# Performance work log

Hardware: AMD Instinct MI355X
Metric: run time of the kernel (lower is better)

Reference implementation:

```python
import jax, jax.numpy as jnp
import numpy as np

NUM_KERNELS = 301
GAMMA = 10.0
SHIFT = float(np.log(2.0))


def shifted_softplus(x):
    return jax.nn.softplus(x) - SHIFT


def setup_inputs() -> dict:
    key = jax.random.key(0)
    k1, k2, k3, k4, k5, k6 = jax.random.split(key, 6)
    N, F, K = 768, 128, NUM_KERNELS
    x = jax.random.normal(k1, (N, F), dtype=jnp.float32)
    # positions scaled to span a realistic distance range vs centers in [0, 30]
    r = jax.random.uniform(k2, (N, 3), dtype=jnp.float32) * 10.0
    W1 = jax.random.normal(k3, (K, F), dtype=jnp.float32) * (1.0 / np.sqrt(K))
    b1 = jax.random.normal(k4, (F,), dtype=jnp.float32) * 0.01
    W2 = jax.random.normal(k5, (F, F), dtype=jnp.float32) * (1.0 / np.sqrt(F))
    b2 = jax.random.normal(k6, (F,), dtype=jnp.float32) * 0.01
    return {"x": x, "r": r, "W1": W1, "b1": b1, "W2": W2, "b2": b2}


def reference(x, r, W1, b1, W2, b2):
    # pairwise Euclidean distances, safe at the zero diagonal
    diff = r[:, None, :] - r[None, :, :]            # [N, N, 3]
    sq = jnp.sum(diff * diff, axis=-1)              # [N, N]
    d = jnp.where(sq > 0, jnp.sqrt(jnp.where(sq > 0, sq, 1.0)), 0.0)
    centers = jnp.linspace(0.0, 30.0, NUM_KERNELS, dtype=jnp.float32)  # [K]
    expanded = jnp.exp(-GAMMA * jnp.square(d[..., None] - centers))    # [N, N, K]
    h = shifted_softplus(expanded @ W1 + b1)        # [N, N, F]
    w = shifted_softplus(h @ W2 + b2)               # [N, N, F]
    o = jnp.einsum('jk,ijk->ik', x, w)              # [N, F]
    return o
```

## Files before the change

### kernel.cpp

```cpp
#include <hip/hip_runtime.h>

#define F        128
#define NN       768
#define KE       192
#define E_STRIDE 200
#define H_STRIDE 136
#define NT       48
#define NBLK     (NT*(NT+1)/2)

#define L2E 1.44269504f
#define LN2 0.69314718f

typedef __attribute__((ext_vector_type(8))) short short8;
typedef __attribute__((ext_vector_type(4))) float floatx4;

__device__ __forceinline__ unsigned short f2bf(float f) {
    union { float f; unsigned u; } v; v.f = f;
    return (unsigned short)((v.u + 0x8000u) >> 16);
}

__device__ __forceinline__ float ssp_zl(float zl2e) {
    float t = exp2f(zl2e);
    float u = __log2f(1.0f + t);
    return fmaf(LN2, u, -LN2);
}

__device__ __forceinline__ void pin(short8& v) { asm volatile("" : "+v"(v)); }

__global__ void prep_w(const float* __restrict__ W1, const float* __restrict__ W2,
                       unsigned short* __restrict__ W1s, unsigned short* __restrict__ W2s,
                       float* __restrict__ out) {
    int idx = blockIdx.x * 256 + threadIdx.x;
    out[idx] = 0.0f;
    if (idx < KE * F) {
        int t = idx & 7, lane = (idx >> 3) & 63, frag = idx >> 9;
        int k = (frag >> 3) * 32 + (lane >> 4) * 8 + t;
        int n = (frag & 7) * 16 + (lane & 15);
        W1s[idx] = f2bf(W1[k * F + n]);
    } else if (idx < KE * F + F * F) {
        int j = idx - KE * F;
        int t = j & 7, lane = (j >> 3) & 63, frag = j >> 9;
        int k = (frag >> 3) * 32 + (lane >> 4) * 8 + t;
        int n = (frag & 7) * 16 + (lane & 15);
        W2s[j] = f2bf(W2[k * F + n]);
    }
}

__global__ __launch_bounds__(256, 2) void cfconv_main(
    const float* __restrict__ x, const float* __restrict__ r,
    const float* __restrict__ b1, const float* __restrict__ b2,
    const unsigned short* __restrict__ W1s, const unsigned short* __restrict__ W2s,
    float* __restrict__ out)
{
    __shared__ __align__(16) unsigned short e_lds[64 * E_STRIDE];
    __shared__ __align__(16) unsigned short h_lds[64 * H_STRIDE];
    __shared__ float d_all[256];
    __shared__ int   klo_all[256];

    const int tid  = threadIdx.x;
    const int lane = tid & 63;
    const int wave = tid >> 6;
    const int quad = lane >> 4;
    const int l15  = lane & 15;

    int b = blockIdx.x;
    int A = (int)((97.0f - sqrtf(9409.0f - 8.0f * (float)b)) * 0.5f);
    while ((A + 1) * (97 - (A + 1)) / 2 <= b) ++A;
    while (A * (97 - A) / 2 > b) --A;
    const int B = A + (b - A * (97 - A) / 2);
    const int Ai0 = A * 16, Bj0 = B * 16;
    const bool diag = (A == B);

    short8 w1f[6][2], w2f[4][2];
    #pragma unroll
    for (int ks = 0; ks < KE / 32; ++ks) {
        w1f[ks][0] = *(const short8*)&W1s[((ks*8 + wave*2 + 0) * 64 + lane) * 8];
        w1f[ks][1] = *(const short8*)&W1s[((ks*8 + wave*2 + 1) * 64 + lane) * 8];
    }
    #pragma unroll
    for (int ks = 0; ks < F / 32; ++ks) {
        w2f[ks][0] = *(const short8*)&W2s[((ks*8 + wave*2 + 0) * 64 + lane) * 8];
        w2f[ks][1] = *(const short8*)&W2s[((ks*8 + wave*2 + 1) * 64 + lane) * 8];
    }
    #pragma unroll
    for (int ks = 0; ks < 6; ++ks) { pin(w1f[ks][0]); pin(w1f[ks][1]); }
    #pragma unroll
    for (int ks = 0; ks < 4; ++ks) { pin(w2f[ks][0]); pin(w2f[ks][1]); }

    {
        int p = tid;
        int gi = Ai0 + (p >> 4), gj = Bj0 + (p & 15);
        float dx = r[gi*3+0] - r[gj*3+0];
        float dy = r[gi*3+1] - r[gj*3+1];
        float dz = r[gi*3+2] - r[gj*3+2];
        float sq = dx*dx + dy*dy + dz*dz;
        float d  = sq > 0.0f ? sqrtf(sq) : 0.0f;
        d_all[p] = d;
        int klo = (int)ceilf(d * 10.0f - 13.0f);
        klo &= ~1;
        klo = klo < 0 ? 0 : (klo > KE - 32 ? KE - 32 : klo);
        klo_all[p] = klo;
    }

    {
        short8 z = 0;
        short8* p8 = (short8*)e_lds;
        for (int c = tid; c < (64 * E_STRIDE) / 8; c += 256) p8[c] = z;
    }

    const int c0 = wave * 32 + l15;
    const int c1 = c0 + 16;
    const float b1L0 = b1[c0] * L2E, b1L1 = b1[c1] * L2E;
    const float b2L0 = b2[c0] * L2E, b2L1 = b2[c1] * L2E;

    float xB0[4], xB1[4];
    #pragma unroll
    for (int rg = 0; rg < 4; ++rg) {
        int gj = Bj0 + quad * 4 + rg;
        xB0[rg] = x[gj * F + c0];
        xB1[rg] = x[gj * F + c1];
    }
    float oB0[4] = {0,0,0,0}, oB1[4] = {0,0,0,0};

    const int rq16 = 16 * ((l15 >> 2) & 3);

    __syncthreads();

    for (int s = 0; s < 4; ++s) {
        {
            int kl = lane & 31;
            for (int rr = wave * 2 + (lane >> 5); rr < 64; rr += 8) {
                if (s > 0)
                    e_lds[rr * E_STRIDE + klo_all[(s-1)*64 + rr] + kl] = 0;
                int p = s * 64 + rr;
                float d = d_all[p];
                int k = klo_all[p] + kl;
                float t = fmaf(-0.1f, (float)k, d);
                float e = exp2f(t * t * (-10.0f * L2E));
                e_lds[rr * E_STRIDE + k] = f2bf(e);
            }
        }
        __syncthreads();

        floatx4 acc[4][2];
        #pragma unroll
        for (int mt = 0; mt < 4; ++mt) { acc[mt][0] = 0; acc[mt][1] = 0; }
        #pragma unroll
        for (int ks = 0; ks < KE / 32; ++ks) {
            short8 af[4];
            #pragma unroll
            for (int mt = 0; mt < 4; ++mt)
                af[mt] = *(const short8*)&e_lds[(mt*16 + l15) * E_STRIDE + ks*32 + quad*8];
            #pragma unroll
            for (int mt = 0; mt < 4; ++mt) {
                acc[mt][0] = __builtin_amdgcn_mfma_f32_16x16x32_bf16(af[mt], w1f[ks][0], acc[mt][0], 0, 0, 0);
                acc[mt][1] = __builtin_amdgcn_mfma_f32_16x16x32_bf16(af[mt], w1f[ks][1], acc[mt][1], 0, 0, 0);
            }
        }

        #pragma unroll
        for (int mt = 0; mt < 4; ++mt) {
            #pragma unroll
            for (int rg = 0; rg < 4; ++rg) {
                int row = mt*16 + quad*4 + rg;
                float h0 = ssp_zl(fmaf(acc[mt][0][rg], L2E, b1L0));
                float h1 = ssp_zl(fmaf(acc[mt][1][rg], L2E, b1L1));
                h_lds[row * H_STRIDE + ((c0 + 16*quad) & 127)] = f2bf(h0);
                h_lds[row * H_STRIDE + ((c1 + 16*quad) & 127)] = f2bf(h1);
            }
        }
        __syncthreads();

        floatx4 acc2[4][2];
        #pragma unroll
        for (int mt = 0; mt < 4; ++mt) { acc2[mt][0] = 0; acc2[mt][1] = 0; }
        #pragma unroll
        for (int ks = 0; ks < F / 32; ++ks) {
            int ko = (ks*32 + quad*8 + rq16) & 127;
            short8 af[4];
            #pragma unroll
            for (int mt = 0; mt < 4; ++mt)
                af[mt] = *(const short8*)&h_lds[(mt*16 + l15) * H_STRIDE + ko];
            #pragma unroll
            for (int mt = 0; mt < 4; ++mt) {
                acc2[mt][0] = __builtin_amdgcn_mfma_f32_16x16x32_bf16(af[mt], w2f[ks][0], acc2[mt][0], 0, 0, 0);
                acc2[mt][1] = __builtin_amdgcn_mfma_f32_16x16x32_bf16(af[mt], w2f[ks][1], acc2[mt][1], 0, 0, 0);
            }
        }

        float xA0[4], xA1[4];
        #pragma unroll
        for (int mt = 0; mt < 4; ++mt) {
            int gi = Ai0 + s*4 + mt;
            xA0[mt] = x[gi * F + c0];
            xA1[mt] = x[gi * F + c1];
        }
        float oA0[4] = {0,0,0,0}, oA1[4] = {0,0,0,0};
        #pragma unroll
        for (int mt = 0; mt < 4; ++mt) {
            #pragma unroll
            for (int rg = 0; rg < 4; ++rg) {
                float w0 = ssp_zl(fmaf(acc2[mt][0][rg], L2E, b2L0));
                float w1 = ssp_zl(fmaf(acc2[mt][1][rg], L2E, b2L1));
                oA0[mt] = fmaf(xB0[rg], w0, oA0[mt]);
                oA1[mt] = fmaf(xB1[rg], w1, oA1[mt]);
                if (!diag) {
                    oB0[rg] = fmaf(xA0[mt], w0, oB0[rg]);
                    oB1[rg] = fmaf(xA1[mt], w1, oB1[rg]);
                }
            }
        }
        #pragma unroll
        for (int mt = 0; mt < 4; ++mt) {
            oA0[mt] += __shfl_xor(oA0[mt], 16, 64); oA0[mt] += __shfl_xor(oA0[mt], 32, 64);
            oA1[mt] += __shfl_xor(oA1[mt], 16, 64); oA1[mt] += __shfl_xor(oA1[mt], 32, 64);
        }
        if (lane < 16) {
            #pragma unroll
            for (int mt = 0; mt < 4; ++mt) {
                int gi = Ai0 + s*4 + mt;
                atomicAdd(&out[gi * F + c0], oA0[mt]);
                atomicAdd(&out[gi * F + c1], oA1[mt]);
            }
        }
    }

    if (!diag) {
        #pragma unroll
        for (int rg = 0; rg < 4; ++rg) {
            int gj = Bj0 + quad * 4 + rg;
            atomicAdd(&out[gj * F + c0], oB0[rg]);
            atomicAdd(&out[gj * F + c1], oB1[rg]);
        }
    }
}

extern "C" void kernel_launch(void* const* d_in, const int* in_sizes, int n_in,
                              void* d_out, int out_size, void* d_ws, size_t ws_size,
                              hipStream_t stream) {
    const float* x  = (const float*)d_in[0];
    const float* r  = (const float*)d_in[1];
    const float* W1 = (const float*)d_in[2];
    const float* b1 = (const float*)d_in[3];
    const float* W2 = (const float*)d_in[4];
    const float* b2 = (const float*)d_in[5];
    float* out = (float*)d_out;

    unsigned short* W1s = (unsigned short*)d_ws;
    unsigned short* W2s = W1s + KE * F;

    prep_w<<<(NN * F) / 256, 256, 0, stream>>>(W1, W2, W1s, W2s, out);
    cfconv_main<<<NBLK, 256, 0, stream>>>(x, r, b1, b2, W1s, W2s, out);
}
```

Baseline: 128.6 us.

## Split each tile-pair block into two halves and coalesce weight prep through LDS

Each 16x16 tile pair is now handled by two blocks, each taking two of the four 64-pair row slices. The grid doubles from 1176 to 2352 blocks to fill the GPU better and cut per-block serial work. The klo table is dropped and klo is recomputed inline, and a barrier is added between the two slices. prep_w now zeroes the output in separate blocks and transposes the weights through shared memory so global reads are coalesced. In exchange, every block still loads the full W1/W2 register fragments and biases, so that setup is repeated twice as often, and the B-side partial sums cause more atomics.

```diff
diff --git a/kernel.cpp b/kernel.cpp
--- a/kernel.cpp
+++ b/kernel.cpp
@@ -6,7 +6,8 @@
 #define E_STRIDE 200
 #define H_STRIDE 136
 #define NT       48
-#define NBLK     (NT*(NT+1)/2)
+#define NPAIR    (NT*(NT+1)/2)
+#define NBLK     (NPAIR*2)
 
 #define L2E 1.44269504f
 #define LN2 0.69314718f
@@ -30,19 +31,31 @@
 __global__ void prep_w(const float* __restrict__ W1, const float* __restrict__ W2,
                        unsigned short* __restrict__ W1s, unsigned short* __restrict__ W2s,
                        float* __restrict__ out) {
-    int idx = blockIdx.x * 256 + threadIdx.x;
-    out[idx] = 0.0f;
-    if (idx < KE * F) {
-        int t = idx & 7, lane = (idx >> 3) & 63, frag = idx >> 9;
-        int k = (frag >> 3) * 32 + (lane >> 4) * 8 + t;
-        int n = (frag & 7) * 16 + (lane & 15);
-        W1s[idx] = f2bf(W1[k * F + n]);
-    } else if (idx < KE * F + F * F) {
-        int j = idx - KE * F;
-        int t = j & 7, lane = (j >> 3) & 63, frag = j >> 9;
-        int k = (frag >> 3) * 32 + (lane >> 4) * 8 + t;
-        int n = (frag & 7) * 16 + (lane & 15);
-        W2s[j] = f2bf(W2[k * F + n]);
+    int bid = blockIdx.x, tid = threadIdx.x;
+    if (bid < 384) {
+        out[bid * 256 + tid] = 0.0f;
+        return;
+    }
+    __shared__ unsigned short lds[32 * 128];
+    int slice = bid - 384;
+    const float* Wsrc;
+    unsigned short* Wdst;
+    int ks;
+    if (slice < 6) { Wsrc = W1; Wdst = W1s; ks = slice; }
+    else           { Wsrc = W2; Wdst = W2s; ks = slice - 6; }
+    #pragma unroll
+    for (int e = 0; e < 16; ++e) {
+        int li = e * 256 + tid;
+        lds[li] = f2bf(Wsrc[ks * 4096 + li]);
+    }
+    __syncthreads();
+    #pragma unroll
+    for (int e = 0; e < 16; ++e) {
+        int oi = e * 256 + tid;
+        int t = oi & 7, lane = (oi >> 3) & 63, frag = oi >> 9;
+        int k_l = (lane >> 4) * 8 + t;
+        int n   = frag * 16 + (lane & 15);
+        Wdst[ks * 4096 + oi] = lds[k_l * 128 + n];
     }
 }
 
@@ -54,8 +67,7 @@
 {
     __shared__ __align__(16) unsigned short e_lds[64 * E_STRIDE];
     __shared__ __align__(16) unsigned short h_lds[64 * H_STRIDE];
-    __shared__ float d_all[256];
-    __shared__ int   klo_all[256];
+    __shared__ float d_all[128];
 
     const int tid  = threadIdx.x;
     const int lane = tid & 63;
@@ -63,7 +75,9 @@
     const int quad = lane >> 4;
     const int l15  = lane & 15;
 
-    int b = blockIdx.x;
+    const int bid  = blockIdx.x;
+    const int half = bid & 1;
+    int b = bid >> 1;
     int A = (int)((97.0f - sqrtf(9409.0f - 8.0f * (float)b)) * 0.5f);
     while ((A + 1) * (97 - (A + 1)) / 2 <= b) ++A;
     while (A * (97 - A) / 2 > b) --A;
@@ -87,19 +101,14 @@
     #pragma unroll
     for (int ks = 0; ks < 4; ++ks) { pin(w2f[ks][0]); pin(w2f[ks][1]); }
 
-    {
-        int p = tid;
-        int gi = Ai0 + (p >> 4), gj = Bj0 + (p & 15);
+    if (tid < 128) {
+        int P = half * 128 + tid;
+        int gi = Ai0 + (P >> 4), gj = Bj0 + (P & 15);
         float dx = r[gi*3+0] - r[gj*3+0];
         float dy = r[gi*3+1] - r[gj*3+1];
         float dz = r[gi*3+2] - r[gj*3+2];
         float sq = dx*dx + dy*dy + dz*dz;
-        float d  = sq > 0.0f ? sqrtf(sq) : 0.0f;
-        d_all[p] = d;
-        int klo = (int)ceilf(d * 10.0f - 13.0f);
-        klo &= ~1;
-        klo = klo < 0 ? 0 : (klo > KE - 32 ? KE - 32 : klo);
-        klo_all[p] = klo;
+        d_all[tid] = sq > 0.0f ? sqrtf(sq) : 0.0f;
     }
 
     {
@@ -126,15 +135,23 @@
 
     __syncthreads();
 
-    for (int s = 0; s < 4; ++s) {
+    #pragma unroll
+    for (int sl = 0; sl < 2; ++sl) {
+        const int s = half * 2 + sl;
+
         {
             int kl = lane & 31;
             for (int rr = wave * 2 + (lane >> 5); rr < 64; rr += 8) {
-                if (s > 0)
-                    e_lds[rr * E_STRIDE + klo_all[(s-1)*64 + rr] + kl] = 0;
-                int p = s * 64 + rr;
-                float d = d_all[p];
-                int k = klo_all[p] + kl;
+                if (sl > 0) {
+                    float dp = d_all[rr];
+                    int kp = ((int)ceilf(dp * 10.0f - 13.0f)) & ~1;
+                    kp = kp < 0 ? 0 : (kp > KE - 32 ? KE - 32 : kp);
+                    e_lds[rr * E_STRIDE + kp + kl] = 0;
+                }
+                float d = d_all[sl * 64 + rr];
+                int klo = ((int)ceilf(d * 10.0f - 13.0f)) & ~1;
+                klo = klo < 0 ? 0 : (klo > KE - 32 ? KE - 32 : klo);
+                int k = klo + kl;
                 float t = fmaf(-0.1f, (float)k, d);
                 float e = exp2f(t * t * (-10.0f * L2E));
                 e_lds[rr * E_STRIDE + k] = f2bf(e);
@@ -223,6 +240,7 @@
                 atomicAdd(&out[gi * F + c1], oA1[mt]);
             }
         }
+        if (sl == 0) __syncthreads();
     }
 
     if (!diag) {
@@ -249,6 +267,6 @@
     unsigned short* W1s = (unsigned short*)d_ws;
     unsigned short* W2s = W1s + KE * F;
 
-    prep_w<<<(NN * F) / 256, 256, 0, stream>>>(W1, W2, W1s, W2s, out);
+    prep_w<<<394, 256, 0, stream>>>(W1, W2, W1s, W2s, out);
     cfconv_main<<<NBLK, 256, 0, stream>>>(x, r, b1, b2, W1s, W2s, out);
 }
```

Result: slower. 131.3 us (+2.1%).
